# Performance work log

Measured on AMD Instinct MI355X. Metric: run time of the kernel, lower is better.

Reference implementation:

```python
import jax, jax.numpy as jnp
import numpy as np
from jax import lax

# 45-tap interpolation filter (fixed buffer in the torch module)
_BASE = np.array([
    -0.00463495665, -0.00363442646, 3.84904063e-18, 0.00576678319, 0.0108358664,
    0.010198079, -9.31747402e-18, -0.0175033181, -0.0317660068, -0.0284531643,
    1.85181518e-17, 0.0442450253, 0.0771733386, 0.067055491, -2.85299239e-17,
    -0.101548683, -0.178708388, -0.160004642, 3.61741232e-17, 0.287940558,
    0.625431459, 0.8970676, 1.00107877, 0.8970676, 0.625431459, 0.287940558,
    3.61741232e-17, -0.160004642, -0.178708388, -0.101548683, -2.85299239e-17,
    0.067055491, 0.0771733386, 0.0442450253, 1.85181518e-17, -0.0284531643,
    -0.0317660068, -0.0175033181, -9.31747402e-18, 0.010198079, 0.0108358664,
    0.00576678319, 3.84904063e-18, -0.00363442646, -0.00463495665], dtype=np.float32)
_COEFF = np.outer(_BASE, _BASE)  # (45, 45), rank-1 separable kernel
_K = _BASE.shape[0]              # 45
_PAD = _K // 2                   # 22
_STRIDE = 4                      # zero-insertion upsample factor
_START = 1                       # start_point offset of nonzero samples


def setup_inputs() -> dict:
    key = jax.random.key(0)
    x = jax.random.normal(key, (16, 8, 128, 128), dtype=jnp.float32)
    return {"x": x}


def reference(x):
    # Equivalent to: zero-insert x at positions 1::4 into a (B,C,4H,4W) grid of
    # zeros, then depthwise conv2d with the 45x45 kernel, padding=22.
    # tensor is materialized): dilated length = 4H-3, placed at offset _START,
    # so pad_lo = 22 + 1 = 23, pad_hi = 22 + (4-1-1) = 24 -> output length 4H.
    B, C, H, W = x.shape
    kernel = jnp.broadcast_to(jnp.asarray(_COEFF, x.dtype), (C, 1, _K, _K))
    pad_lo = _PAD + _START                    # 23
    pad_hi = _PAD + (_STRIDE - 1 - _START)    # 24
    out = lax.conv_general_dilated(
        x, kernel,
        window_strides=(1, 1),
        padding=((pad_lo, pad_hi), (pad_lo, pad_hi)),
        lhs_dilation=(_STRIDE, _STRIDE),
        dimension_numbers=("NCHW", "OIHW", "NCHW"),
        feature_group_count=C,
    )
    return out  # (B, C, 4H, 4W)
```

## Files before the change

kernel.cpp:

```cpp
#include <hip/hip_runtime.h>

constexpr float BASE48[48] = {
    -0.00463495665f, -0.00363442646f, 3.84904063e-18f, 0.00576678319f, 0.0108358664f,
    0.010198079f, -9.31747402e-18f, -0.0175033181f, -0.0317660068f, -0.0284531643f,
    1.85181518e-17f, 0.0442450253f, 0.0771733386f, 0.067055491f, -2.85299239e-17f,
    -0.101548683f, -0.178708388f, -0.160004642f, 3.61741232e-17f, 0.287940558f,
    0.625431459f, 0.8970676f, 1.00107877f, 0.8970676f, 0.625431459f, 0.287940558f,
    3.61741232e-17f, -0.160004642f, -0.178708388f, -0.101548683f, -2.85299239e-17f,
    0.067055491f, 0.0771733386f, 0.0442450253f, 1.85181518e-17f, -0.0284531643f,
    -0.0317660068f, -0.0175033181f, -9.31747402e-18f, 0.010198079f, 0.0108358664f,
    0.00576678319f, 3.84904063e-18f, -0.00363442646f, -0.00463495665f,
    0.0f, 0.0f, 0.0f
};

__device__ __forceinline__ void fma4(float4& a, float w, const float4& v) {
    a.x = fmaf(w, v.x, a.x);
    a.y = fmaf(w, v.y, a.y);
    a.z = fmaf(w, v.z, a.z);
    a.w = fmaf(w, v.w, a.w);
}

__launch_bounds__(256)
__global__ void upfirdn4_sep_kernel(const float* __restrict__ x,
                                    float* __restrict__ out) {
    constexpr int H = 128, W = 128, OW = 512, OH = 512;

    __shared__ float in_s[27][28];
    __shared__ float tmp[27][64];

    const int tid = threadIdx.x;
    const int bc  = blockIdx.z;
    const int OX  = blockIdx.x * 64;
    const int OY  = blockIdx.y * 64;
    const int I0x = (OX >> 2) - 5;
    const int I0y = (OY >> 2) - 5;

    const float* xb = x + (size_t)bc * (H * W);

    for (int t = tid; t < 27 * 28; t += 256) {
        int r = t / 28;
        int c = t - r * 28;
        int iy = I0y + r;
        int ix = I0x + c;
        float v = 0.0f;
        if ((unsigned)iy < (unsigned)H && (unsigned)ix < (unsigned)W)
            v = xb[iy * W + ix];
        in_s[r][c] = v;
    }
    __syncthreads();

    for (int t = tid; t < 27 * 16; t += 256) {
        int row = t >> 4;
        int m   = t & 15;
        float a0 = 0.f, a1 = 0.f, a2 = 0.f, a3 = 0.f;
#pragma unroll
        for (int j = 0; j < 12; ++j) {
            float v = in_s[row][m + j];
            a0 = fmaf(BASE48[4 * j + 3], v, a0);
            a1 = fmaf(BASE48[4 * j + 2], v, a1);
            a2 = fmaf(BASE48[4 * j + 1], v, a2);
            a3 = fmaf(BASE48[4 * j + 0], v, a3);
        }
        *(float4*)&tmp[row][m << 2] = make_float4(a0, a1, a2, a3);
    }
    __syncthreads();

    {
        int m  = tid >> 4;
        int oc = (tid & 15) << 2;
        float4 acc0 = {0, 0, 0, 0}, acc1 = {0, 0, 0, 0};
        float4 acc2 = {0, 0, 0, 0}, acc3 = {0, 0, 0, 0};
#pragma unroll
        for (int j = 0; j < 12; ++j) {
            float4 v = *(const float4*)&tmp[m + j][oc];
            fma4(acc0, BASE48[4 * j + 3], v);
            fma4(acc1, BASE48[4 * j + 2], v);
            fma4(acc2, BASE48[4 * j + 1], v);
            fma4(acc3, BASE48[4 * j + 0], v);
        }
        size_t base = (size_t)bc * (OH * OW) + (size_t)(OY + (m << 2)) * OW + (OX + oc);
        *(float4*)&out[base]          = acc0;
        *(float4*)&out[base + OW]     = acc1;
        *(float4*)&out[base + 2 * OW] = acc2;
        *(float4*)&out[base + 3 * OW] = acc3;
    }
}

extern "C" void kernel_launch(void* const* d_in, const int* in_sizes, int n_in,
                              void* d_out, int out_size, void* d_ws, size_t ws_size,
                              hipStream_t stream) {
    const float* x = (const float*)d_in[0];
    float* out = (float*)d_out;
    dim3 grid(8, 8, 128);
    dim3 block(256);
    upfirdn4_sep_kernel<<<grid, block, 0, stream>>>(x, out);
}
```

Baseline: 31.86 us.

## Enlarge output tile to 128x128 and use nontemporal stores

Doubles the per-block output tile in each dimension, so each block loads a 43x44 input halo and computes four output rows of float4 per thread, reducing the halo recomputation overhead of the horizontal pass. Output writes switch to nontemporal stores to avoid polluting cache with the large streaming output. The trade-off is a quarter as many blocks and more LDS per block, which can lower occupancy and latency hiding.

```diff
diff --git a/kernel.cpp b/kernel.cpp
--- a/kernel.cpp
+++ b/kernel.cpp
@@ -1,4 +1,6 @@
 #include <hip/hip_runtime.h>
+
+typedef float v4f __attribute__((ext_vector_type(4)));
 
 constexpr float BASE48[48] = {
     -0.00463495665f, -0.00363442646f, 3.84904063e-18f, 0.00576678319f, 0.0108358664f,
@@ -13,7 +15,7 @@
     0.0f, 0.0f, 0.0f
 };
 
-__device__ __forceinline__ void fma4(float4& a, float w, const float4& v) {
+__device__ __forceinline__ void fma4(v4f& a, float w, const v4f& v) {
     a.x = fmaf(w, v.x, a.x);
     a.y = fmaf(w, v.y, a.y);
     a.z = fmaf(w, v.z, a.z);
@@ -24,22 +26,23 @@
 __global__ void upfirdn4_sep_kernel(const float* __restrict__ x,
                                     float* __restrict__ out) {
     constexpr int H = 128, W = 128, OW = 512, OH = 512;
+    constexpr int TSTRIDE = 132;
 
-    __shared__ float in_s[27][28];
-    __shared__ float tmp[27][64];
+    __shared__ float in_s[43][44];
+    __shared__ float tmp[43][TSTRIDE];
 
     const int tid = threadIdx.x;
     const int bc  = blockIdx.z;
-    const int OX  = blockIdx.x * 64;
-    const int OY  = blockIdx.y * 64;
+    const int OX  = blockIdx.x * 128;
+    const int OY  = blockIdx.y * 128;
     const int I0x = (OX >> 2) - 5;
     const int I0y = (OY >> 2) - 5;
 
     const float* xb = x + (size_t)bc * (H * W);
 
-    for (int t = tid; t < 27 * 28; t += 256) {
-        int r = t / 28;
-        int c = t - r * 28;
+    for (int t = tid; t < 43 * 44; t += 256) {
+        int r = t / 44;
+        int c = t - r * 44;
         int iy = I0y + r;
         int ix = I0x + c;
         float v = 0.0f;
@@ -49,9 +52,9 @@
     }
     __syncthreads();
 
-    for (int t = tid; t < 27 * 16; t += 256) {
-        int row = t >> 4;
-        int m   = t & 15;
+    for (int t = tid; t < 43 * 32; t += 256) {
+        int row = t >> 5;
+        int m   = t & 31;
         float a0 = 0.f, a1 = 0.f, a2 = 0.f, a3 = 0.f;
 #pragma unroll
         for (int j = 0; j < 12; ++j) {
@@ -61,28 +64,31 @@
             a2 = fmaf(BASE48[4 * j + 1], v, a2);
             a3 = fmaf(BASE48[4 * j + 0], v, a3);
         }
-        *(float4*)&tmp[row][m << 2] = make_float4(a0, a1, a2, a3);
+        v4f r4 = {a0, a1, a2, a3};
+        *(v4f*)&tmp[row][m << 2] = r4;
     }
     __syncthreads();
 
-    {
-        int m  = tid >> 4;
-        int oc = (tid & 15) << 2;
-        float4 acc0 = {0, 0, 0, 0}, acc1 = {0, 0, 0, 0};
-        float4 acc2 = {0, 0, 0, 0}, acc3 = {0, 0, 0, 0};
+#pragma unroll
+    for (int it = 0; it < 4; ++it) {
+        int pidx = tid + it * 256;
+        int py = pidx >> 5;
+        int oc = (pidx & 31) << 2;
+        v4f acc0 = {0, 0, 0, 0}, acc1 = {0, 0, 0, 0};
+        v4f acc2 = {0, 0, 0, 0}, acc3 = {0, 0, 0, 0};
 #pragma unroll
         for (int j = 0; j < 12; ++j) {
-            float4 v = *(const float4*)&tmp[m + j][oc];
+            v4f v = *(const v4f*)&tmp[py + j][oc];
             fma4(acc0, BASE48[4 * j + 3], v);
             fma4(acc1, BASE48[4 * j + 2], v);
             fma4(acc2, BASE48[4 * j + 1], v);
             fma4(acc3, BASE48[4 * j + 0], v);
         }
-        size_t base = (size_t)bc * (OH * OW) + (size_t)(OY + (m << 2)) * OW + (OX + oc);
-        *(float4*)&out[base]          = acc0;
-        *(float4*)&out[base + OW]     = acc1;
-        *(float4*)&out[base + 2 * OW] = acc2;
-        *(float4*)&out[base + 3 * OW] = acc3;
+        size_t base = (size_t)bc * (OH * OW) + (size_t)(OY + (py << 2)) * OW + (OX + oc);
+        __builtin_nontemporal_store(acc0, (v4f*)&out[base]);
+        __builtin_nontemporal_store(acc1, (v4f*)&out[base + OW]);
+        __builtin_nontemporal_store(acc2, (v4f*)&out[base + 2 * OW]);
+        __builtin_nontemporal_store(acc3, (v4f*)&out[base + 3 * OW]);
     }
 }
 
@@ -91,7 +97,7 @@
                               hipStream_t stream) {
     const float* x = (const float*)d_in[0];
     float* out = (float*)d_out;
-    dim3 grid(8, 8, 128);
+    dim3 grid(4, 4, 128);
     dim3 block(256);
     upfirdn4_sep_kernel<<<grid, block, 0, stream>>>(x, out);
 }
```

Result: slower. 42.16 us (+32.3%).

## Swap pass order: vertical filter from global, horizontal from registers

Applied to the files above, without the earlier changes.

Reorders the separable polyphase filter so the vertical pass reads input directly from global memory into a 64x27 shared intermediate. The horizontal pass then works on a per-thread register window and writes 16 contiguous outputs per row. This drops the input staging buffer and one barrier, and adds an interior fast path without bounds checks. In exchange, global loads are strided and redundant, and the store pattern changes.

```diff
diff --git a/kernel.cpp b/kernel.cpp
--- a/kernel.cpp
+++ b/kernel.cpp
@@ -1,4 +1,6 @@
 #include <hip/hip_runtime.h>
+
+typedef float v4f __attribute__((ext_vector_type(4)));
 
 constexpr float BASE48[48] = {
     -0.00463495665f, -0.00363442646f, 3.84904063e-18f, 0.00576678319f, 0.0108358664f,
@@ -13,20 +15,12 @@
     0.0f, 0.0f, 0.0f
 };
 
-__device__ __forceinline__ void fma4(float4& a, float w, const float4& v) {
-    a.x = fmaf(w, v.x, a.x);
-    a.y = fmaf(w, v.y, a.y);
-    a.z = fmaf(w, v.z, a.z);
-    a.w = fmaf(w, v.w, a.w);
-}
-
 __launch_bounds__(256)
-__global__ void upfirdn4_sep_kernel(const float* __restrict__ x,
-                                    float* __restrict__ out) {
+__global__ void upfirdn4_vh_kernel(const float* __restrict__ x,
+                                   float* __restrict__ out) {
     constexpr int H = 128, W = 128, OW = 512, OH = 512;
 
-    __shared__ float in_s[27][28];
-    __shared__ float tmp[27][64];
+    __shared__ float vtmp[64][28];
 
     const int tid = threadIdx.x;
     const int bc  = blockIdx.z;
@@ -37,52 +31,70 @@
 
     const float* xb = x + (size_t)bc * (H * W);
 
-    for (int t = tid; t < 27 * 28; t += 256) {
-        int r = t / 28;
-        int c = t - r * 28;
-        int iy = I0y + r;
-        int ix = I0x + c;
-        float v = 0.0f;
-        if ((unsigned)iy < (unsigned)H && (unsigned)ix < (unsigned)W)
-            v = xb[iy * W + ix];
-        in_s[r][c] = v;
-    }
-    __syncthreads();
-
-    for (int t = tid; t < 27 * 16; t += 256) {
-        int row = t >> 4;
-        int m   = t & 15;
+    const bool interior = (I0x >= 0) & (I0x + 27 <= W) & (I0y >= 0) & (I0y + 27 <= H);
+#pragma unroll
+    for (int it = 0; it < 2; ++it) {
+        int t  = tid + it * 256;
+        int c  = t & 31;
+        int rg = t >> 5;
+        int cc = c < 27 ? c : 26;
         float a0 = 0.f, a1 = 0.f, a2 = 0.f, a3 = 0.f;
+        if (interior) {
+            const float* p = xb + (I0y + rg) * W + (I0x + cc);
 #pragma unroll
-        for (int j = 0; j < 12; ++j) {
-            float v = in_s[row][m + j];
-            a0 = fmaf(BASE48[4 * j + 3], v, a0);
-            a1 = fmaf(BASE48[4 * j + 2], v, a1);
-            a2 = fmaf(BASE48[4 * j + 1], v, a2);
-            a3 = fmaf(BASE48[4 * j + 0], v, a3);
+            for (int j = 0; j < 12; ++j) {
+                float v = p[j * W];
+                a0 = fmaf(BASE48[4 * j + 3], v, a0);
+                a1 = fmaf(BASE48[4 * j + 2], v, a1);
+                a2 = fmaf(BASE48[4 * j + 1], v, a2);
+                a3 = fmaf(BASE48[4 * j + 0], v, a3);
+            }
+        } else {
+            int ix = I0x + cc;
+#pragma unroll
+            for (int j = 0; j < 12; ++j) {
+                int iy = I0y + rg + j;
+                float v = 0.0f;
+                if ((unsigned)iy < (unsigned)H && (unsigned)ix < (unsigned)W)
+                    v = xb[iy * W + ix];
+                a0 = fmaf(BASE48[4 * j + 3], v, a0);
+                a1 = fmaf(BASE48[4 * j + 2], v, a1);
+                a2 = fmaf(BASE48[4 * j + 1], v, a2);
+                a3 = fmaf(BASE48[4 * j + 0], v, a3);
+            }
         }
-        *(float4*)&tmp[row][m << 2] = make_float4(a0, a1, a2, a3);
+        if (c < 27) {
+            vtmp[4 * rg + 0][c] = a0;
+            vtmp[4 * rg + 1][c] = a1;
+            vtmp[4 * rg + 2][c] = a2;
+            vtmp[4 * rg + 3][c] = a3;
+        }
     }
     __syncthreads();
 
     {
-        int m  = tid >> 4;
-        int oc = (tid & 15) << 2;
-        float4 acc0 = {0, 0, 0, 0}, acc1 = {0, 0, 0, 0};
-        float4 acc2 = {0, 0, 0, 0}, acc3 = {0, 0, 0, 0};
+        int r = tid >> 2;
+        int g = tid & 3;
+        float win[16];
+        *(v4f*)&win[0]  = *(const v4f*)&vtmp[r][4 * g + 0];
+        *(v4f*)&win[4]  = *(const v4f*)&vtmp[r][4 * g + 4];
+        *(v4f*)&win[8]  = *(const v4f*)&vtmp[r][4 * g + 8];
+        *(v4f*)&win[12] = *(const v4f*)&vtmp[r][4 * g + 12];
+        size_t rowbase = (size_t)bc * (OH * OW) + (size_t)(OY + r) * OW + (OX + 16 * g);
 #pragma unroll
-        for (int j = 0; j < 12; ++j) {
-            float4 v = *(const float4*)&tmp[m + j][oc];
-            fma4(acc0, BASE48[4 * j + 3], v);
-            fma4(acc1, BASE48[4 * j + 2], v);
-            fma4(acc2, BASE48[4 * j + 1], v);
-            fma4(acc3, BASE48[4 * j + 0], v);
+        for (int k = 0; k < 4; ++k) {
+            float b0 = 0.f, b1 = 0.f, b2 = 0.f, b3 = 0.f;
+#pragma unroll
+            for (int j = 0; j < 12; ++j) {
+                float v = win[k + j];
+                b0 = fmaf(BASE48[4 * j + 3], v, b0);
+                b1 = fmaf(BASE48[4 * j + 2], v, b1);
+                b2 = fmaf(BASE48[4 * j + 1], v, b2);
+                b3 = fmaf(BASE48[4 * j + 0], v, b3);
+            }
+            v4f r4 = {b0, b1, b2, b3};
+            *(v4f*)&out[rowbase + 4 * k] = r4;
         }
-        size_t base = (size_t)bc * (OH * OW) + (size_t)(OY + (m << 2)) * OW + (OX + oc);
-        *(float4*)&out[base]          = acc0;
-        *(float4*)&out[base + OW]     = acc1;
-        *(float4*)&out[base + 2 * OW] = acc2;
-        *(float4*)&out[base + 3 * OW] = acc3;
     }
 }
 
@@ -93,5 +105,5 @@
     float* out = (float*)d_out;
     dim3 grid(8, 8, 128);
     dim3 block(256);
-    upfirdn4_sep_kernel<<<grid, block, 0, stream>>>(x, out);
+    upfirdn4_vh_kernel<<<grid, block, 0, stream>>>(x, out);
 }
```

New measurement: 50.00 us. 56.9% more time.
